# Performance work log

Measured on AMD Instinct MI355X. Metric: run time of the kernel, lower is better.

Reference implementation:

```python
import jax, jax.numpy as jnp
import numpy as np
from jax import lax

ANCHOR_AREAS = (128.0**2, 256.0**2, 512.0**2)
ASPECT_RATIOS = (0.5, 1.0, 2.0)
STRIDE = 32.0                      # resnet backbone: get_orig_stat maps fm -> input via x*32
PRE_NMS_TOP_N = 2000
POST_NMS_TOP_N = 100
NMS_IOU_T = 0.7
SCORE_T = 0.1
MIN_SCALE = 0.01
BBOX_XFORM_CLIP = float(np.log(1000.0 / 16.0))


def make_anchors(H, W):
    # anchors laid out in (H, W, A) order to match the offset permutation below
    sizes = []
    for area in ANCHOR_AREAS:
        for r in ASPECT_RATIOS:          # aspect_ratio = w / h
            sizes.append((np.sqrt(area * r), np.sqrt(area / r)))
    sizes = jnp.asarray(np.asarray(sizes, dtype=np.float32))  # [A, 2] (w, h)
    cy = (jnp.arange(H, dtype=jnp.float32) + 0.5) * STRIDE
    cx = (jnp.arange(W, dtype=jnp.float32) + 0.5) * STRIDE
    cyg, cxg = jnp.meshgrid(cy, cx, indexing='ij')             # [H, W]
    cxg = cxg[:, :, None]
    cyg = cyg[:, :, None]
    w = sizes[:, 0]
    h = sizes[:, 1]
    anchors = jnp.stack([cxg - w / 2, cyg - h / 2, cxg + w / 2, cyg + h / 2], axis=-1)
    return anchors.reshape(-1, 4)                              # [H*W*A, 4] xyxy


def decode_boxes(anchors, offsets):
    # anchors [N,4], offsets [B,N,4] (tx, ty, tw, th) -> boxes [B,N,4] xyxy
    wa = anchors[:, 2] - anchors[:, 0]
    ha = anchors[:, 3] - anchors[:, 1]
    cxa = anchors[:, 0] + 0.5 * wa
    cya = anchors[:, 1] + 0.5 * ha
    tx, ty = offsets[..., 0], offsets[..., 1]
    tw = jnp.minimum(offsets[..., 2], BBOX_XFORM_CLIP)
    th = jnp.minimum(offsets[..., 3], BBOX_XFORM_CLIP)
    px = tx * wa + cxa
    py = ty * ha + cya
    pw = jnp.exp(tw) * wa
    ph = jnp.exp(th) * ha
    return jnp.stack([px - pw / 2, py - ph / 2, px + pw / 2, py + ph / 2], axis=-1)


def box_iou(a, b):
    area_a = (a[:, 2] - a[:, 0]) * (a[:, 3] - a[:, 1])
    area_b = (b[:, 2] - b[:, 0]) * (b[:, 3] - b[:, 1])
    lt = jnp.maximum(a[:, None, :2], b[None, :, :2])
    rb = jnp.minimum(a[:, None, 2:], b[None, :, 2:])
    wh = jnp.clip(rb - lt, 0.0)
    inter = wh[..., 0] * wh[..., 1]
    return inter / (area_a[:, None] + area_b[None, :] - inter + 1e-9)


def nms_single(boxes, scores):
    # boxes [P,4] sorted by descending score; invalid entries carry score -1
    P = boxes.shape[0]
    iou = box_iou(boxes, boxes)
    idx = jnp.arange(P)

    def body(i, keep):
        sup = (iou[i] > NMS_IOU_T) & (idx > i)
        return jnp.where(keep[i], keep & (~sup), keep)

    keep = lax.stop_gradient(lax.fori_loop(0, P, body, scores > 0.0))
    kept_scores = jnp.where(keep, scores, -1.0)
    top_s, top_i = lax.top_k(kept_scores, POST_NMS_TOP_N)
    return boxes[top_i], top_s


def rpn_forward(features, W1, b1, W2, b2, W3, b3):
    B, Cin, H, W = features.shape
    A = W3.shape[0]
    # 3x3 sliding conv + ReLU
    t = lax.conv_general_dilated(
        features, W1, window_strides=(1, 1), padding='SAME',
        dimension_numbers=('NCHW', 'OIHW', 'NCHW'))
    t = jax.nn.relu(t + b1[None, :, None, None])
    # 1x1 sibling heads as channel contractions
    offs = jnp.einsum('bchw,oc->bohw', t, W2) + b2[None, :, None, None]   # [B, A*4, H, W]
    logits = jnp.einsum('bchw,oc->bohw', t, W3) + b3[None, :, None, None]  # [B, A, H, W]
    # reorder to per-anchor layout (H, W, A)
    offs = offs.reshape(B, A, 4, H, W).transpose(0, 3, 4, 1, 2).reshape(B, -1, 4)
    scores = jax.nn.sigmoid(logits.transpose(0, 2, 3, 1).reshape(B, -1))  # [B, N]
    anchors = make_anchors(H, W)
    boxes = decode_boxes(anchors, offs)                                    # [B, N, 4]
    # clip to image boundary (handle_cross_boundary_boxes during testing)
    img_w, img_h = W * STRIDE, H * STRIDE
    boxes = jnp.stack([
        jnp.clip(boxes[..., 0], 0.0, img_w),
        jnp.clip(boxes[..., 1], 0.0, img_h),
        jnp.clip(boxes[..., 2], 0.0, img_w),
        jnp.clip(boxes[..., 3], 0.0, img_h)], axis=-1)
    # score-threshold + min-scale filtering
    bw = boxes[..., 2] - boxes[..., 0]
    bh = boxes[..., 3] - boxes[..., 1]
    valid = (scores >= SCORE_T) & (bw > MIN_SCALE * img_w) & (bh > MIN_SCALE * img_h)
    masked = jnp.where(valid, scores, -1.0)
    # pre-NMS top-k, then per-image NMS + post-NMS top-n
    top_s, top_i = lax.top_k(masked, PRE_NMS_TOP_N)                        # [B, P]
    top_boxes = jnp.take_along_axis(boxes, top_i[..., None], axis=1)       # [B, P, 4]
    out_boxes, out_scores = jax.vmap(nms_single)(top_boxes, top_s)
    return out_boxes, out_scores                                           # [B,100,4], [B,100]


def setup_inputs() -> dict:
    key = jax.random.key(0)
    ks = jax.random.split(key, 4)
    B, Cin, H, W = 8, 1024, 50, 50
    A = 9
    C = 512
    return {
        'features': jax.random.normal(ks[0], (B, Cin, H, W), jnp.float32),
        'W1': jax.random.normal(ks[1], (C, Cin, 3, 3), jnp.float32) * 0.01,
        'b1': jnp.zeros((C,), jnp.float32),
        'W2': jax.random.normal(ks[2], (A * 4, C), jnp.float32) * 0.01,
        'b2': jnp.zeros((A * 4,), jnp.float32),
        'W3': jax.random.normal(ks[3], (A, C), jnp.float32) * 0.01,
        'b3': jnp.zeros((A,), jnp.float32),
    }


def reference(features, W1, b1, W2, b2, W3, b3):
    return rpn_forward(features, W1, b1, W2, b2, W3, b3)
```

## Files before the change

kernel.cpp:

```cpp
#include <hip/hip_runtime.h>
#include <cstdint>

#define NB 8
#define CIN 1024
#define HDIM 50
#define WDIM 50
#define COUT 512
#define NA 9
#define NANCH (HDIM*WDIM*NA)
#define PRE_N 2000
#define POST_N 100

typedef __attribute__((ext_vector_type(8))) short bf16x8;
typedef __attribute__((ext_vector_type(4))) float f32x4;
typedef __attribute__((ext_vector_type(16))) float f32x16;
typedef __attribute__((ext_vector_type(8))) unsigned short ushort8v;

constexpr size_t TPLANE    = 20578304;
constexpr size_t OFF_TPH   = 0;
constexpr size_t OFF_TPL   = 20578304;
constexpr size_t OFF_BOXES = 41156608;
constexpr size_t OFF_KEYS  = 44036608;
constexpr size_t OFF_TBOX  = 45476608;
constexpr size_t OFF_TS    = 45732608;
constexpr size_t OFF_SUP   = 45796608;
constexpr size_t QDIM      = 2976;
constexpr size_t PLSTRIDE  = QDIM * 8;
constexpr size_t PPLANE    = 48758784;
constexpr size_t OFF_PH    = 49892864;
constexpr size_t OFF_PL    = OFF_PH + PPLANE;
constexpr size_t WPLANE    = 9437184;
constexpr size_t OFF_WH    = 147410432;
constexpr size_t OFF_WL    = OFF_WH + WPLANE;

__device__ __forceinline__ void split2bf16(float v, unsigned short &hi, unsigned short &lo) {
    unsigned int u = __float_as_uint(v);
    unsigned int r = u + 0x7FFFu + ((u >> 16) & 1u);
    hi = (unsigned short)(r >> 16);
    float hf = __uint_as_float(((unsigned int)hi) << 16);
    float lf = v - hf;
    unsigned int u2 = __float_as_uint(lf);
    unsigned int r2 = u2 + 0x7FFFu + ((u2 >> 16) & 1u);
    lo = (unsigned short)(r2 >> 16);
}

__device__ __forceinline__ void gl_lds(const unsigned short* g, unsigned short* l) {
    __builtin_amdgcn_global_load_lds(
        (const __attribute__((address_space(1))) unsigned int*)(const void*)g,
        (__attribute__((address_space(3))) unsigned int*)(void*)l,
        16, 0, 0);
}

__global__ __launch_bounds__(256) void prep_all(const float* __restrict__ f,
                                                const float* __restrict__ W1,
                                                unsigned short* __restrict__ Ph,
                                                unsigned short* __restrict__ Pl,
                                                unsigned short* __restrict__ Wh,
                                                unsigned short* __restrict__ Wl) {
    int blk = blockIdx.x;
    if (blk < 5952) {
        int id = blk * 256 + threadIdx.x;
        int q = id % (int)QDIM; int r = id / (int)QDIM;
        int cic = r % 64; int b = r / 64;
        int pp = q - 53;
        int rr = pp / 52, cc = pp - rr * 52;
        int h = rr - 1, w = cc - 1;
        bool inb = (pp >= 0) && (pp < 2704) && (h >= 0) && (h < HDIM) && (w >= 0) && (w < WDIM);
        ushort8v hv0, lv0, hv1, lv1;
#pragma unroll
        for (int j = 0; j < 16; ++j) {
            float v = 0.f;
            if (inb) v = f[(((size_t)b * CIN + cic * 16 + j) * HDIM + h) * WDIM + w];
            unsigned short hi, lo;
            split2bf16(v, hi, lo);
            if (j < 8) { hv0[j] = hi; lv0[j] = lo; }
            else       { hv1[j - 8] = hi; lv1[j - 8] = lo; }
        }
        size_t b0 = ((size_t)((b * 64 + cic) * 2 + 0)) * PLSTRIDE + (size_t)q * 8;
        size_t b1 = ((size_t)((b * 64 + cic) * 2 + 1)) * PLSTRIDE + (size_t)q * 8;
        *(ushort8v*)&Ph[b0] = hv0;
        *(ushort8v*)&Ph[b1] = hv1;
        *(ushort8v*)&Pl[b0] = lv0;
        *(ushort8v*)&Pl[b1] = lv1;
    } else {
        int id = (blk - 5952) * 256 + threadIdx.x;
        int co = id % 64; int r = id / 64;
        int cic = r % 64; int cot = r / 64;
        int cog = cot * 64 + co;
        const float* src = W1 + ((size_t)cog * CIN + cic * 16) * 9;
        float v[144];
#pragma unroll
        for (int i = 0; i < 36; ++i) {
            float4 x = ((const float4*)src)[i];
            v[i * 4 + 0] = x.x; v[i * 4 + 1] = x.y; v[i * 4 + 2] = x.z; v[i * 4 + 3] = x.w;
        }
#pragma unroll
        for (int tap = 0; tap < 9; ++tap) {
            ushort8v hv0, lv0, hv1, lv1;
#pragma unroll
            for (int j = 0; j < 16; ++j) {
                unsigned short hi, lo;
                split2bf16(v[j * 9 + tap], hi, lo);
                if (j < 8) { hv0[j] = hi; lv0[j] = lo; }
                else       { hv1[j - 8] = hi; lv1[j - 8] = lo; }
            }
            size_t base = (((size_t)(cot * 64 + cic) * 9 + tap) * 2) * 512;
            *(ushort8v*)&Wh[base + co * 8]       = hv0;
            *(ushort8v*)&Wh[base + 512 + co * 8] = hv1;
            *(ushort8v*)&Wl[base + co * 8]       = lv0;
            *(ushort8v*)&Wl[base + 512 + co * 8] = lv1;
        }
    }
}


#define LOADA(SET_, SRC_, TG_)                                                       \
    do {                                                                             \
        _Pragma("unroll") for (int tl_ = 0; tl_ < 3; ++tl_) {                        \
            const int dlt_ = ((TG_) - 1) * 52 + (tl_ - 1);                           \
            _Pragma("unroll") for (int jm_ = 0; jm_ < 2; ++jm_) {                    \
                int ad_ = ((wv * 2 + jm_) * 32 + lm + dlt_ + 53) * 8;                \
                SET_[tl_][jm_][0] = *(const bf16x8*)&(SRC_)[lk * 3072 + ad_];        \
                SET_[tl_][jm_][1] = *(const bf16x8*)&(SRC_)[(2 + lk) * 3072 + ad_];  \
            }                                                                        \
        }                                                                            \
    } while (0)

#define LOADB(B_, BB_, TL_)                                                          \
    do {                                                                             \
        _Pragma("unroll") for (int jn_ = 0; jn_ < 2; ++jn_) {                        \
            int bd_ = (TL_) * 1024 + lk * 512 + (jn_ * 32 + lm) * 8;                 \
            B_[jn_][0] = *(const bf16x8*)&(BB_)[bd_];                                \
            B_[jn_][1] = *(const bf16x8*)&(BB_)[3072 + bd_];                         \
        }                                                                            \
    } while (0)

#define MFMA12A(SET_, TL_, B_)                                                       \
    do {                                                                             \
        _Pragma("unroll") for (int s_ = 0; s_ < 3; ++s_)                             \
        _Pragma("unroll") for (int jm_ = 0; jm_ < 2; ++jm_)                          \
        _Pragma("unroll") for (int jn_ = 0; jn_ < 2; ++jn_) {                        \
            const bf16x8 &av_ = (s_ == 2) ? SET_[TL_][jm_][1] : SET_[TL_][jm_][0];   \
            const bf16x8 &bv_ = (s_ == 1) ? B_[jn_][1] : B_[jn_][0];                 \
            acc[jm_][jn_] = __builtin_amdgcn_mfma_f32_32x32x16_bf16(                 \
                av_, bv_, acc[jm_][jn_], 0, 0, 0);                                   \
        }                                                                            \
    } while (0)

#define PHASE(CUR_, NXT_, CIC_, TG_, PRESRC_, NTG_, STAGEON_)                        \
    do {                                                                             \
        const int bbuf_ = ((CIC_) + (TG_)) & 1;                                      \
        const unsigned short* bB_ = Bbase + bbuf_ * 6144;                            \
        if ((STAGEON_) || (TG_) < 2) {                                               \
            int cicb_ = ((TG_) == 2) ? (CIC_) + 1 : (CIC_);                          \
            int tgn_  = ((TG_) == 2) ? 0 : (TG_) + 1;                                \
            _Pragma("unroll") for (int j_ = 0; j_ < 3; ++j_)                         \
                stageB(bbuf_ ^ 1, cicb_, tgn_, wv * 3 + j_);                         \
        }                                                                            \
        if (STAGEON_) {                                                              \
            if ((TG_) == 0) {                                                        \
                _Pragma("unroll") for (int j_ = 0; j_ < 3; ++j_)                     \
                    stageA((((CIC_) & 1) ^ 1), (CIC_) + 1, wv * 3 + j_);             \
            } else if ((TG_) == 1) {                                                 \
                _Pragma("unroll") for (int j_ = 0; j_ < 2; ++j_)                     \
                    stageA((((CIC_) & 1) ^ 1), (CIC_) + 1, 12 + wv * 2 + j_);        \
            } else {                                                                 \
                stageA((((CIC_) & 1) ^ 1), (CIC_) + 1, 20 + wv);                     \
            }                                                                        \
        }                                                                            \
        bf16x8 b0_[2][2], b1_[2][2];                                                 \
        LOADB(b0_, bB_, 0);                                                          \
        __builtin_amdgcn_s_setprio(1);                                               \
        LOADB(b1_, bB_, 1);                                                          \
        MFMA12A(CUR_, 0, b0_);                                                       \
        LOADB(b0_, bB_, 2);                                                          \
        if ((STAGEON_) || (TG_) < 2) LOADA(NXT_, PRESRC_, NTG_);                     \
        MFMA12A(CUR_, 1, b1_);                                                       \
        MFMA12A(CUR_, 2, b0_);                                                       \
        __builtin_amdgcn_s_setprio(0);                                               \
        if (STAGEON_) {                                                              \
            const int nv_ = ((TG_) == 0) ? 6 : ((TG_) == 1) ? 5 : 4;                 \
            __builtin_amdgcn_sched_group_barrier(0x070, nv_, 0);                     \
            __builtin_amdgcn_sched_group_barrier(0x100, 8, 0);                       \
            _Pragma("unroll") for (int g_ = 0; g_ < 8; ++g_) {                       \
                __builtin_amdgcn_sched_group_barrier(0x008, 3, 0);                   \
                __builtin_amdgcn_sched_group_barrier(0x100, 2, 0);                   \
            }                                                                        \
            __builtin_amdgcn_sched_group_barrier(0x008, 12, 0);                      \
        }                                                                            \
        __syncthreads();                                                             \
    } while (0)

#define DO_CIC(CUR_, NXT_, CIC_, STAGEON_)                                           \
    do {                                                                             \
        const unsigned short* bAc_ = Abase + ((CIC_) & 1) * 12288;                   \
        const unsigned short* bAn_ = Abase + (((CIC_) & 1) ^ 1) * 12288;             \
        PHASE(CUR_, NXT_, CIC_, 0, bAc_, 1, STAGEON_);                               \
        PHASE(NXT_, CUR_, CIC_, 1, bAc_, 2, STAGEON_);                               \
        PHASE(CUR_, NXT_, CIC_, 2, bAn_, 0, STAGEON_);                               \
    } while (0)

__global__ __launch_bounds__(256, 2) void conv_mfma(const unsigned short* __restrict__ FPh,
                                                    const unsigned short* __restrict__ FPl,
                                                    const unsigned short* __restrict__ WPh,
                                                    const unsigned short* __restrict__ WPl,
                                                    const float* __restrict__ b1,
                                                    unsigned short* __restrict__ Tph,
                                                    unsigned short* __restrict__ Tpl) {
    extern __shared__ unsigned short smem[];
    unsigned short* const Abase = smem;
    unsigned short* const Bbase = smem + 24576;

    int blk = blockIdx.x;
    int logical = (blk & 7) * 88 + (blk >> 3);
    int cot = logical & 7;
    int ptile = (logical >> 3) % 11;
    int b = logical / 88;
    int co0 = cot * 64;
    int P0 = 32 + ptile * 256;

    int t = threadIdx.x, wv = t >> 6, ln = t & 63;
    int lm = ln & 31, lk = ln >> 5;

    f32x16 acc[2][2];
#pragma unroll
    for (int jm = 0; jm < 2; ++jm)
#pragma unroll
        for (int jn = 0; jn < 2; ++jn)
#pragma unroll
            for (int rg = 0; rg < 16; ++rg) acc[jm][jn][rg] = 0.f;

    auto stageA = [&](int buf, int cic, int ci) {
        int r = (ci < 20) ? (ci & 3) : (ci - 20);
        int s = (ci < 20) ? (ci >> 2) : 5;
        int hl = r >> 1, lkc = r & 1;
        const unsigned short* pl = hl ? FPl : FPh;
        const unsigned short* src = pl
            + ((size_t)((b * 64 + cic) * 2 + lkc)) * PLSTRIDE
            + (size_t)P0 * 8 + s * 512 + ln * 8;
        gl_lds(src, &Abase[buf * 12288 + r * 3072 + s * 512]);
    };
    auto stageB = [&](int buf, int cic, int tg, int c) {
        int hl = c / 6, j = c % 6;
        const unsigned short* pl = hl ? WPl : WPh;
        const unsigned short* src = pl + (size_t)(cot * 64 + cic) * 9216
            + (size_t)(tg * 6 + j) * 512 + ln * 8;
        gl_lds(src, &Bbase[buf * 6144 + hl * 3072 + j * 512]);
    };

#pragma unroll
    for (int k = 0; k < 9; ++k) {
        int id = wv * 9 + k;
        if (id < 24) stageA(0, 0, id);
        else         stageB(0, 0, 0, id - 24);
    }
    __syncthreads();

    bf16x8 aX[3][2][2], aY[3][2][2];
    LOADA(aX, Abase, 0);

#pragma unroll 1
    for (int cc = 0; cc < 31; ++cc) {
        DO_CIC(aX, aY, 2 * cc,     1);
        DO_CIC(aY, aX, 2 * cc + 1, 1);
    }
    DO_CIC(aX, aY, 62, 1);
    DO_CIC(aY, aX, 63, 0);

#pragma unroll
    for (int jn = 0; jn < 2; ++jn) {
        int co = co0 + jn * 32 + lm;
        float bv = b1[co];
#pragma unroll
        for (int jm = 0; jm < 2; ++jm) {
#pragma unroll
            for (int rg = 0; rg < 16; ++rg) {
                int mrow = (rg & 3) + 8 * (rg >> 2) + 4 * lk;
                int pp = P0 + (wv * 2 + jm) * 32 + mrow;
                int rr = pp / 52, cc = pp - rr * 52;
                int h = rr - 1, w = cc - 1;
                if ((unsigned)h < HDIM && (unsigned)w < WDIM) {
                    float v = fmaxf(acc[jm][jn][rg] + bv, 0.f);
                    unsigned short hi, lo;
                    split2bf16(v, hi, lo);
                    int px = b * 2500 + h * 50 + w;
                    size_t sa = (((((size_t)(px >> 7) * 16 + (co >> 5)) * 8 + ((px >> 4) & 7)) * 4
                                  + ((co >> 3) & 3)) * 16 + (px & 15)) * 8 + (co & 7);
                    Tph[sa] = hi;
                    Tpl[sa] = lo;
                }
            }
        }
    }
}

__global__ __launch_bounds__(256) void proj_decode_mfma(const unsigned short* __restrict__ Tph,
                                                        const unsigned short* __restrict__ Tpl,
                                                        const float* __restrict__ W2,
                                                        const float* __restrict__ b2,
                                                        const float* __restrict__ W3,
                                                        const float* __restrict__ b3,
                                                        float* __restrict__ boxes,
                                                        unsigned long long* __restrict__ keys) {
    __shared__ unsigned short sTh[4096], sTl[4096];
    __shared__ unsigned short sWh[1536], sWl[1536];
    __shared__ float pout[128 * 46];

    int blk = blockIdx.x;
    int px0 = blk * 128;
    int t = threadIdx.x, wv = t >> 6, ln = t & 63;
    int lm = ln & 15, q = ln >> 4;

    f32x4 acc[2][3];
#pragma unroll
    for (int jm = 0; jm < 2; ++jm)
#pragma unroll
        for (int nf = 0; nf < 3; ++nf) acc[jm][nf] = (f32x4){0.f, 0.f, 0.f, 0.f};

#pragma unroll 1
    for (int cc16 = 0; cc16 < 16; ++cc16) {
        __syncthreads();
        size_t base = ((size_t)blk * 16 + cc16) * 4096;
        if (wv == 0) {
#pragma unroll
            for (int s = 0; s < 4; ++s) gl_lds(Tph + base + s * 512 + ln * 8, &sTh[s * 512]);
        } else if (wv == 1) {
#pragma unroll
            for (int s = 4; s < 8; ++s) gl_lds(Tph + base + s * 512 + ln * 8, &sTh[s * 512]);
        } else if (wv == 2) {
#pragma unroll
            for (int s = 0; s < 4; ++s) gl_lds(Tpl + base + s * 512 + ln * 8, &sTl[s * 512]);
        } else {
#pragma unroll
            for (int s = 4; s < 8; ++s) gl_lds(Tpl + base + s * 512 + ln * 8, &sTl[s * 512]);
        }
        int c0 = cc16 * 32;
        for (int idx = t; idx < 1536; idx += 256) {
            int o = idx >> 5, ci = idx & 31;
            float v = 0.f;
            if (o < 36) v = W2[o * 512 + c0 + ci];
            else if (o < 45) v = W3[(o - 36) * 512 + c0 + ci];
            unsigned short hi, lo;
            split2bf16(v, hi, lo);
            int ad = (((o >> 4) * 4 + (ci >> 3)) * 16 + (o & 15)) * 8 + (ci & 7);
            sWh[ad] = hi; sWl[ad] = lo;
        }
        __syncthreads();

        bf16x8 a[2][2], bb[3][2];
#pragma unroll
        for (int jm = 0; jm < 2; ++jm) {
            int mf = wv * 2 + jm;
            int ad = ((mf * 4 + q) * 16 + lm) * 8;
            a[jm][0] = *(const bf16x8*)&sTh[ad];
            a[jm][1] = *(const bf16x8*)&sTl[ad];
        }
#pragma unroll
        for (int nf = 0; nf < 3; ++nf) {
            int ad = ((nf * 4 + q) * 16 + lm) * 8;
            bb[nf][0] = *(const bf16x8*)&sWh[ad];
            bb[nf][1] = *(const bf16x8*)&sWl[ad];
        }
#pragma unroll
        for (int jm = 0; jm < 2; ++jm)
#pragma unroll
            for (int nf = 0; nf < 3; ++nf) {
                acc[jm][nf] = __builtin_amdgcn_mfma_f32_16x16x32_bf16(a[jm][0], bb[nf][0], acc[jm][nf], 0, 0, 0);
                acc[jm][nf] = __builtin_amdgcn_mfma_f32_16x16x32_bf16(a[jm][0], bb[nf][1], acc[jm][nf], 0, 0, 0);
                acc[jm][nf] = __builtin_amdgcn_mfma_f32_16x16x32_bf16(a[jm][1], bb[nf][0], acc[jm][nf], 0, 0, 0);
            }
    }
    __syncthreads();
#pragma unroll
    for (int jm = 0; jm < 2; ++jm)
#pragma unroll
        for (int nf = 0; nf < 3; ++nf) {
            int o = nf * 16 + lm;
            if (o < 45) {
                float bias = (o < 36) ? b2[o] : b3[o - 36];
#pragma unroll
                for (int rg = 0; rg < 4; ++rg) {
                    int pxl = (wv * 2 + jm) * 16 + q * 4 + rg;
                    pout[pxl * 46 + o] = acc[jm][nf][rg] + bias;
                }
            }
        }
    __syncthreads();

    const float AW[9] = {90.50966799187809f, 128.0f, 181.01933598375618f,
                         181.01933598375618f, 256.0f, 362.03867196751236f,
                         362.03867196751236f, 512.0f, 724.0773439350247f};
    const float AH[9] = {181.01933598375618f, 128.0f, 90.50966799187809f,
                         362.03867196751236f, 256.0f, 181.01933598375618f,
                         724.0773439350247f, 512.0f, 362.03867196751236f};
    const float CLIPV = 4.135166556742356f;
    const float IMG = 1600.0f;

    for (int it = t; it < 128 * 9; it += 256) {
        int pxl = it / 9, a = it - pxl * 9;
        int pxg = px0 + pxl;
        if (pxg >= 20000) continue;
        int b = pxg / 2500, rem = pxg % 2500;
        int h = rem / 50, w = rem % 50;

        float tx = pout[pxl * 46 + a * 4 + 0];
        float ty = pout[pxl * 46 + a * 4 + 1];
        float tw = pout[pxl * 46 + a * 4 + 2];
        float th = pout[pxl * 46 + a * 4 + 3];
        float lg = pout[pxl * 46 + 36 + a];

        float s = 1.0f / (1.0f + expf(-lg));

        float cx = ((float)w + 0.5f) * 32.0f;
        float cy = ((float)h + 0.5f) * 32.0f;
        float x1a = cx - 0.5f * AW[a];
        float x2a = cx + 0.5f * AW[a];
        float y1a = cy - 0.5f * AH[a];
        float y2a = cy + 0.5f * AH[a];
        float waf = x2a - x1a;
        float haf = y2a - y1a;
        float cxa = x1a + 0.5f * waf;
        float cya = y1a + 0.5f * haf;

        float twc = tw < CLIPV ? tw : CLIPV;
        float thc = th < CLIPV ? th : CLIPV;
        float pxc = tx * waf + cxa;
        float pyc = ty * haf + cya;
        float pw  = expf(twc) * waf;
        float ph  = expf(thc) * haf;

        float x1 = pxc - 0.5f * pw;
        float y1 = pyc - 0.5f * ph;
        float x2 = pxc + 0.5f * pw;
        float y2 = pyc + 0.5f * ph;
        x1 = fminf(fmaxf(x1, 0.f), IMG);
        y1 = fminf(fmaxf(y1, 0.f), IMG);
        x2 = fminf(fmaxf(x2, 0.f), IMG);
        y2 = fminf(fmaxf(y2, 0.f), IMG);

        float bw = x2 - x1, bh = y2 - y1;
        bool valid = (s >= 0.1f) && (bw > 16.0f) && (bh > 16.0f);
        float m = valid ? s : -1.0f;

        int idx = (h * WDIM + w) * NA + a;
        size_t gi = (size_t)b * NANCH + idx;
        ((float4*)boxes)[gi] = make_float4(x1, y1, x2, y2);
        unsigned int u = __float_as_uint(m);
        unsigned int k32 = (u & 0x80000000u) ? ~u : (u | 0x80000000u);
        keys[gi] = ((unsigned long long)k32 << 15) | (unsigned long long)(32767 - idx);
    }
}

__global__ __launch_bounds__(1024) void select_sort_kernel(const unsigned long long* __restrict__ keys,
                                                           const float* __restrict__ boxes,
                                                           float* __restrict__ top_boxes,
                                                           float* __restrict__ top_s) {
    int b = blockIdx.x;
    int t = threadIdx.x;
    int wv = t >> 6;
    const unsigned long long* kb = keys + (size_t)b * NANCH;

    __shared__ unsigned int whist[16][256];
    __shared__ unsigned int hist[256];
    __shared__ int s_chosen, s_rnew, s_done;
    __shared__ unsigned int s_cnt;
    __shared__ unsigned long long skeys[2048];

    const int widths[6] = {8, 8, 8, 8, 8, 7};
    unsigned long long prefix = 0;
    int bitsdone = 0;
    int r = PRE_N;

    if (t == 0) s_done = 0;

    for (int p = 0; p < 6; ++p) {
        int width = widths[p];
        int bins = 1 << width;
        int shift = 47 - bitsdone - width;
        for (int i = t; i < 16 * 256; i += 1024) ((unsigned int*)whist)[i] = 0;
        __syncthreads();
        for (int i = t; i < NANCH; i += 1024) {
            unsigned long long k = kb[i];
            if ((k >> (47 - bitsdone)) == prefix)
                atomicAdd(&whist[wv][(unsigned)((k >> shift) & (unsigned long long)(bins - 1))], 1u);
        }
        __syncthreads();
        if (t < bins) {
            unsigned int s = 0;
#pragma unroll
            for (int w = 0; w < 16; ++w) s += whist[w][t];
            hist[t] = s;
        }
        __syncthreads();
        if (t == 0) {
            int acc = 0, chosen = 0, rnew = 1;
            for (int d = bins - 1; d >= 0; --d) {
                int hv = (int)hist[d];
                if (acc + hv >= r) {
                    chosen = d; rnew = r - acc;
                    if ((PRE_N - r) + acc + hv <= 2048) s_done = 1;
                    break;
                }
                acc += hv;
            }
            s_chosen = chosen;
            s_rnew = rnew;
        }
        __syncthreads();
        prefix = (prefix << width) | (unsigned long long)s_chosen;
        bitsdone += width;
        r = s_rnew;
        __syncthreads();
        if (s_done) break;
    }
    unsigned long long Kst = prefix << (47 - bitsdone);

    if (t == 0) s_cnt = 0;
    __syncthreads();
    for (int i = t; i < NANCH; i += 1024) {
        unsigned long long k = kb[i];
        if (k >= Kst) {
            unsigned int p = atomicAdd(&s_cnt, 1u);
            if (p < 2048) skeys[p] = k;
        }
    }
    __syncthreads();
    unsigned int cnt = s_cnt;
    for (int i = t; i < 2048; i += 1024)
        if (i >= (int)cnt) skeys[i] = 0ull;
    for (int k = 2; k <= 2048; k <<= 1) {
        for (int j = k >> 1; j > 0; j >>= 1) {
            __syncthreads();
            for (int i = t; i < 2048; i += 1024) {
                int l = i ^ j;
                if (l > i) {
                    unsigned long long a = skeys[i], c = skeys[l];
                    bool up = ((i & k) == 0);
                    if (up ? (a < c) : (a > c)) { skeys[i] = c; skeys[l] = a; }
                }
            }
        }
    }
    __syncthreads();
    for (int i = t; i < PRE_N; i += 1024) {
        unsigned long long k = skeys[i];
        unsigned int k32 = (unsigned int)(k >> 15);
        float m = (k32 & 0x80000000u) ? __uint_as_float(k32 & 0x7FFFFFFFu)
                                      : __uint_as_float(~k32);
        unsigned int idx = 32767u - (unsigned int)(k & 32767ull);
        size_t gi = (size_t)b * NANCH + idx;
        top_s[b * PRE_N + i] = m;
        ((float4*)top_boxes)[b * PRE_N + i] = ((const float4*)boxes)[gi];
    }
}

__global__ __launch_bounds__(256) void sup_kernel(const float* __restrict__ top_boxes,
                                                  unsigned long long* __restrict__ supm) {
    int blk = blockIdx.x;
    int b = blk / 125;
    int chunk = blk % 125;
    int t = threadIdx.x;

    __shared__ float bx1[PRE_N], by1[PRE_N], bx2[PRE_N], by2[PRE_N];
    for (int i = t; i < PRE_N; i += 256) {
        float4 v = ((const float4*)top_boxes)[b * PRE_N + i];
        bx1[i] = v.x; by1[i] = v.y; bx2[i] = v.z; by2[i] = v.w;
    }
    __syncthreads();

    int wave = t >> 6, lane = t & 63;
    for (int rr = 0; rr < 4; ++rr) {
        int i = chunk * 16 + wave * 4 + rr;
        float ax1 = bx1[i], ay1 = by1[i], ax2 = bx2[i], ay2 = by2[i];
        float aarea = (ax2 - ax1) * (ay2 - ay1);
        for (int jw = 0; jw < 32; ++jw) {
            int j = jw * 64 + lane;
            bool sup = false;
            if (j > i && j < PRE_N) {
                float jx1 = bx1[j], jy1 = by1[j], jx2 = bx2[j], jy2 = by2[j];
                float ix1 = fmaxf(ax1, jx1), iy1 = fmaxf(ay1, jy1);
                float ix2 = fminf(ax2, jx2), iy2 = fminf(ay2, jy2);
                float iw = fmaxf(ix2 - ix1, 0.f);
                float ih = fmaxf(iy2 - iy1, 0.f);
                float inter = iw * ih;
                float barea = (jx2 - jx1) * (jy2 - jy1);
                float iou = inter / (aarea + barea - inter + 1e-9f);
                sup = iou > 0.7f;
            }
            unsigned long long m = __ballot(sup);
            if (lane == 0) supm[((size_t)b * PRE_N + i) * 32 + jw] = m;
        }
    }
}

__global__ __launch_bounds__(256) void nms_fin_kernel(const float* __restrict__ top_s,
                                                      const unsigned long long* __restrict__ supm,
                                                      const float* __restrict__ top_boxes,
                                                      float* __restrict__ out) {
    int b = blockIdx.x;
    int t = threadIdx.x;
    __shared__ unsigned int kw[64];
    __shared__ int wpre[65];

    if (t < 64) {
        int lane = t;
        unsigned int alive = 0;
        for (int q = 0; q < 32; ++q) {
            int i = lane * 32 + q;
            if (i < PRE_N && top_s[b * PRE_N + i] > 0.f) alive |= (1u << q);
        }
        const unsigned long long* sm = supm + (size_t)b * PRE_N * 32;
        const unsigned int* sup32 = (const unsigned int*)sm;

        for (int tt = 0; tt < 32; ++tt) {
            unsigned int alo = __shfl(alive, 2 * tt);
            unsigned int ahi = __shfl(alive, 2 * tt + 1);
            unsigned long long talive = (unsigned long long)alo | ((unsigned long long)ahi << 32);
            int i_row = tt * 64 + lane;
            unsigned long long rm = (i_row < PRE_N) ? sm[(size_t)i_row * 32 + tt] : 0ull;

            unsigned long long kept = 0, rem = talive;
            while (rem) {
                int j = __builtin_ctzll(rem);
                kept |= (1ull << j);
                unsigned long long rmj = __shfl(rm, j);
                rem &= ~rmj;
                rem &= ~(1ull << j);
            }

            unsigned int oracc = 0;
            unsigned long long kk = kept;
            while (kk) {
                int j0 = __builtin_ctzll(kk); kk &= kk - 1;
                int j1 = -1, j2 = -1, j3 = -1, j4 = -1, j5 = -1, j6 = -1, j7 = -1;
                if (kk) { j1 = __builtin_ctzll(kk); kk &= kk - 1; }
                if (kk) { j2 = __builtin_ctzll(kk); kk &= kk - 1; }
                if (kk) { j3 = __builtin_ctzll(kk); kk &= kk - 1; }
                if (kk) { j4 = __builtin_ctzll(kk); kk &= kk - 1; }
                if (kk) { j5 = __builtin_ctzll(kk); kk &= kk - 1; }
                if (kk) { j6 = __builtin_ctzll(kk); kk &= kk - 1; }
                if (kk) { j7 = __builtin_ctzll(kk); kk &= kk - 1; }
                unsigned int v0 = sup32[(size_t)(tt * 64 + j0) * 64 + lane];
                unsigned int v1 = (j1 >= 0) ? sup32[(size_t)(tt * 64 + j1) * 64 + lane] : 0u;
                unsigned int v2 = (j2 >= 0) ? sup32[(size_t)(tt * 64 + j2) * 64 + lane] : 0u;
                unsigned int v3 = (j3 >= 0) ? sup32[(size_t)(tt * 64 + j3) * 64 + lane] : 0u;
                unsigned int v4 = (j4 >= 0) ? sup32[(size_t)(tt * 64 + j4) * 64 + lane] : 0u;
                unsigned int v5 = (j5 >= 0) ? sup32[(size_t)(tt * 64 + j5) * 64 + lane] : 0u;
                unsigned int v6 = (j6 >= 0) ? sup32[(size_t)(tt * 64 + j6) * 64 + lane] : 0u;
                unsigned int v7 = (j7 >= 0) ? sup32[(size_t)(tt * 64 + j7) * 64 + lane] : 0u;
                oracc |= (v0 | v1) | (v2 | v3) | (v4 | v5) | (v6 | v7);
            }
            alive &= ~oracc;
            if (lane == 2 * tt)     alive = (unsigned int)kept;
            if (lane == 2 * tt + 1) alive = (unsigned int)(kept >> 32);
        }
        kw[lane] = alive;
    }
    __syncthreads();
    if (t == 0) {
        int run = 0;
        for (int w = 0; w < 64; ++w) { wpre[w] = run; run += __popc(kw[w]); }
        wpre[64] = run;
    }
    __syncthreads();
    int total = wpre[64];
    float* out_boxes  = out;
    float* out_scores = out + NB * POST_N * 4;
    for (int i = t; i < PRE_N; i += 256) {
        unsigned int w = kw[i >> 5];
        bool kept = (w >> (i & 31)) & 1u;
        int rk = wpre[i >> 5] + __popc(w & ((1u << (i & 31)) - 1u));
        int pos = kept ? rk : total + (i - rk);
        if (pos < POST_N) {
            out_scores[b * POST_N + pos] = kept ? top_s[b * PRE_N + i] : -1.0f;
            ((float4*)out_boxes)[b * POST_N + pos] = ((const float4*)top_boxes)[b * PRE_N + i];
        }
    }
}

extern "C" void kernel_launch(void* const* d_in, const int* in_sizes, int n_in,
                              void* d_out, int out_size, void* d_ws, size_t ws_size,
                              hipStream_t stream) {
    const float* features = (const float*)d_in[0];
    const float* W1 = (const float*)d_in[1];
    const float* b1 = (const float*)d_in[2];
    const float* W2 = (const float*)d_in[3];
    const float* b2 = (const float*)d_in[4];
    const float* W3 = (const float*)d_in[5];
    const float* b3 = (const float*)d_in[6];
    float* out = (float*)d_out;
    char* ws = (char*)d_ws;

    unsigned short* Tph = (unsigned short*)(ws + OFF_TPH);
    unsigned short* Tpl = (unsigned short*)(ws + OFF_TPL);
    float* boxes   = (float*)(ws + OFF_BOXES);
    unsigned long long* keys = (unsigned long long*)(ws + OFF_KEYS);
    float* top_boxes = (float*)(ws + OFF_TBOX);
    float* top_s     = (float*)(ws + OFF_TS);
    unsigned long long* supm = (unsigned long long*)(ws + OFF_SUP);
    unsigned short* FPh = (unsigned short*)(ws + OFF_PH);
    unsigned short* FPl = (unsigned short*)(ws + OFF_PL);
    unsigned short* WPh = (unsigned short*)(ws + OFF_WH);
    unsigned short* WPl = (unsigned short*)(ws + OFF_WL);

    static bool conv_attr_set = false;
    if (!conv_attr_set) {
        hipFuncSetAttribute(reinterpret_cast<const void*>(&conv_mfma),
                            hipFuncAttributeMaxDynamicSharedMemorySize, 73728);
        conv_attr_set = true;
    }

    prep_all<<<6080, 256, 0, stream>>>(features, W1, FPh, FPl, WPh, WPl);
    conv_mfma<<<704, 256, 73728, stream>>>(FPh, FPl, WPh, WPl, b1, Tph, Tpl);
    proj_decode_mfma<<<157, 256, 0, stream>>>(Tph, Tpl, W2, b2, W3, b3, boxes, keys);
    select_sort_kernel<<<NB, 1024, 0, stream>>>(keys, boxes, top_boxes, top_s);
    sup_kernel<<<NB * 125, 256, 0, stream>>>(top_boxes, supm);
    nms_fin_kernel<<<NB, 256, 0, stream>>>(top_s, supm, top_boxes, out);
}
```

Before: 973.7 us.

## Load conv weights directly from global into registers, drop LDS staging of B

```diff
diff --git a/kernel.cpp b/kernel.cpp
--- a/kernel.cpp
+++ b/kernel.cpp
@@ -126,15 +126,6 @@
         }                                                                            \
     } while (0)
 
-#define LOADB(B_, BB_, TL_)                                                          \
-    do {                                                                             \
-        _Pragma("unroll") for (int jn_ = 0; jn_ < 2; ++jn_) {                        \
-            int bd_ = (TL_) * 1024 + lk * 512 + (jn_ * 32 + lm) * 8;                 \
-            B_[jn_][0] = *(const bf16x8*)&(BB_)[bd_];                                \
-            B_[jn_][1] = *(const bf16x8*)&(BB_)[3072 + bd_];                         \
-        }                                                                            \
-    } while (0)
-
 #define MFMA12A(SET_, TL_, B_)                                                       \
     do {                                                                             \
         _Pragma("unroll") for (int s_ = 0; s_ < 3; ++s_)                             \
@@ -147,57 +138,45 @@
         }                                                                            \
     } while (0)
 
-#define PHASE(CUR_, NXT_, CIC_, TG_, PRESRC_, NTG_, STAGEON_)                        \
+#define PHASEV(CUR_, NXT_, CIC_, TG_, PRESRC_, NTG_, DOA_, DOLOADA_)                 \
     do {                                                                             \
-        const int bbuf_ = ((CIC_) + (TG_)) & 1;                                      \
-        const unsigned short* bB_ = Bbase + bbuf_ * 6144;                            \
-        if ((STAGEON_) || (TG_) < 2) {                                               \
-            int cicb_ = ((TG_) == 2) ? (CIC_) + 1 : (CIC_);                          \
-            int tgn_  = ((TG_) == 2) ? 0 : (TG_) + 1;                                \
+        size_t wo_ = (size_t)(cot * 64 + (CIC_)) * 9216 + (size_t)((TG_) * 3072);    \
+        bf16x8 bb_[3][2][2];                                                         \
+        _Pragma("unroll") for (int tl_ = 0; tl_ < 3; ++tl_)                          \
+        _Pragma("unroll") for (int jn_ = 0; jn_ < 2; ++jn_) {                        \
+            size_t o_ = wo_ + (size_t)(tl_ * 1024 + lk * 512 + (jn_ * 32 + lm) * 8); \
+            bb_[tl_][jn_][0] = *(const bf16x8*)&WPh[o_];                             \
+            bb_[tl_][jn_][1] = *(const bf16x8*)&WPl[o_];                             \
+        }                                                                            \
+        if (DOA_) {                                                                  \
             _Pragma("unroll") for (int j_ = 0; j_ < 3; ++j_)                         \
-                stageB(bbuf_ ^ 1, cicb_, tgn_, wv * 3 + j_);                         \
+                stageA(abn_, (CIC_) + 1, (TG_) * 12 + wv * 3 + j_);                  \
         }                                                                            \
-        if (STAGEON_) {                                                              \
-            if ((TG_) == 0) {                                                        \
-                _Pragma("unroll") for (int j_ = 0; j_ < 3; ++j_)                     \
-                    stageA((((CIC_) & 1) ^ 1), (CIC_) + 1, wv * 3 + j_);             \
-            } else if ((TG_) == 1) {                                                 \
-                _Pragma("unroll") for (int j_ = 0; j_ < 2; ++j_)                     \
-                    stageA((((CIC_) & 1) ^ 1), (CIC_) + 1, 12 + wv * 2 + j_);        \
-            } else {                                                                 \
-                stageA((((CIC_) & 1) ^ 1), (CIC_) + 1, 20 + wv);                     \
+        __builtin_amdgcn_s_setprio(1);                                               \
+        MFMA12A(CUR_, 0, bb_[0]);                                                    \
+        if (DOLOADA_) LOADA(NXT_, PRESRC_, NTG_);                                    \
+        MFMA12A(CUR_, 1, bb_[1]);                                                    \
+        MFMA12A(CUR_, 2, bb_[2]);                                                    \
+        __builtin_amdgcn_s_setprio(0);                                               \
+        if (DOLOADA_) {                                                              \
+                                         \
+            __builtin_amdgcn_sched_group_barrier(0x070, (DOA_) ? 27 : 24, 0);        \
+            _Pragma("unroll") for (int g_ = 0; g_ < 12; ++g_) {                      \
+                __builtin_amdgcn_sched_group_barrier(0x008, 3, 0);                   \
+                __builtin_amdgcn_sched_group_barrier(0x100, 1, 0);                   \
             }                                                                        \
         }                                                                            \
-        bf16x8 b0_[2][2], b1_[2][2];                                                 \
-        LOADB(b0_, bB_, 0);                                                          \
-        __builtin_amdgcn_s_setprio(1);                                               \
-        LOADB(b1_, bB_, 1);                                                          \
-        MFMA12A(CUR_, 0, b0_);                                                       \
-        LOADB(b0_, bB_, 2);                                                          \
-        if ((STAGEON_) || (TG_) < 2) LOADA(NXT_, PRESRC_, NTG_);                     \
-        MFMA12A(CUR_, 1, b1_);                                                       \
-        MFMA12A(CUR_, 2, b0_);                                                       \
-        __builtin_amdgcn_s_setprio(0);                                               \
-        if (STAGEON_) {                                                              \
-            const int nv_ = ((TG_) == 0) ? 6 : ((TG_) == 1) ? 5 : 4;                 \
-            __builtin_amdgcn_sched_group_barrier(0x070, nv_, 0);                     \
-            __builtin_amdgcn_sched_group_barrier(0x100, 8, 0);                       \
-            _Pragma("unroll") for (int g_ = 0; g_ < 8; ++g_) {                       \
-                __builtin_amdgcn_sched_group_barrier(0x008, 3, 0);                   \
-                __builtin_amdgcn_sched_group_barrier(0x100, 2, 0);                   \
-            }                                                                        \
-            __builtin_amdgcn_sched_group_barrier(0x008, 12, 0);                      \
-        }                                                                            \
-        __syncthreads();                                                             \
     } while (0)
 
-#define DO_CIC(CUR_, NXT_, CIC_, STAGEON_)                                           \
+#define DO_CICV(CUR_, NXT_, CIC_, STAGEON_, LOADLAST_)                               \
     do {                                                                             \
         const unsigned short* bAc_ = Abase + ((CIC_) & 1) * 12288;                   \
         const unsigned short* bAn_ = Abase + (((CIC_) & 1) ^ 1) * 12288;             \
-        PHASE(CUR_, NXT_, CIC_, 0, bAc_, 1, STAGEON_);                               \
-        PHASE(NXT_, CUR_, CIC_, 1, bAc_, 2, STAGEON_);                               \
-        PHASE(CUR_, NXT_, CIC_, 2, bAn_, 0, STAGEON_);                               \
+        const int abn_ = ((CIC_) & 1) ^ 1;                                           \
+        PHASEV(CUR_, NXT_, CIC_, 0, bAc_, 1, STAGEON_, 1);                           \
+        PHASEV(NXT_, CUR_, CIC_, 1, bAc_, 2, STAGEON_, 1);                           \
+        __syncthreads();                                                             \
+        PHASEV(CUR_, NXT_, CIC_, 2, bAn_, 0, 0, LOADLAST_);                          \
     } while (0)
 
 __global__ __launch_bounds__(256, 2) void conv_mfma(const unsigned short* __restrict__ FPh,
@@ -207,9 +186,8 @@
                                                     const float* __restrict__ b1,
                                                     unsigned short* __restrict__ Tph,
                                                     unsigned short* __restrict__ Tpl) {
-    extern __shared__ unsigned short smem[];
-    unsigned short* const Abase = smem;
-    unsigned short* const Bbase = smem + 24576;
+    __shared__ unsigned short sA[2][4][3072];
+    unsigned short* const Abase = &sA[0][0][0];
 
     int blk = blockIdx.x;
     int logical = (blk & 7) * 88 + (blk >> 3);
@@ -231,8 +209,7 @@
             for (int rg = 0; rg < 16; ++rg) acc[jm][jn][rg] = 0.f;
 
     auto stageA = [&](int buf, int cic, int ci) {
-        int r = (ci < 20) ? (ci & 3) : (ci - 20);
-        int s = (ci < 20) ? (ci >> 2) : 5;
+        int r = ci & 3, s = ci >> 2;
         int hl = r >> 1, lkc = r & 1;
         const unsigned short* pl = hl ? FPl : FPh;
         const unsigned short* src = pl
@@ -240,20 +217,9 @@
             + (size_t)P0 * 8 + s * 512 + ln * 8;
         gl_lds(src, &Abase[buf * 12288 + r * 3072 + s * 512]);
     };
-    auto stageB = [&](int buf, int cic, int tg, int c) {
-        int hl = c / 6, j = c % 6;
-        const unsigned short* pl = hl ? WPl : WPh;
-        const unsigned short* src = pl + (size_t)(cot * 64 + cic) * 9216
-            + (size_t)(tg * 6 + j) * 512 + ln * 8;
-        gl_lds(src, &Bbase[buf * 6144 + hl * 3072 + j * 512]);
-    };
-
-#pragma unroll
-    for (int k = 0; k < 9; ++k) {
-        int id = wv * 9 + k;
-        if (id < 24) stageA(0, 0, id);
-        else         stageB(0, 0, 0, id - 24);
-    }
+
+#pragma unroll
+    for (int k = 0; k < 6; ++k) stageA(0, 0, wv * 6 + k);
     __syncthreads();
 
     bf16x8 aX[3][2][2], aY[3][2][2];
@@ -261,11 +227,11 @@
 
 #pragma unroll 1
     for (int cc = 0; cc < 31; ++cc) {
-        DO_CIC(aX, aY, 2 * cc,     1);
-        DO_CIC(aY, aX, 2 * cc + 1, 1);
-    }
-    DO_CIC(aX, aY, 62, 1);
-    DO_CIC(aY, aX, 63, 0);
+        DO_CICV(aX, aY, 2 * cc,     1, 1);
+        DO_CICV(aY, aX, 2 * cc + 1, 1, 1);
+    }
+    DO_CICV(aX, aY, 62, 1, 1);
+    DO_CICV(aY, aX, 63, 0, 0);
 
 #pragma unroll
     for (int jn = 0; jn < 2; ++jn) {
@@ -703,15 +669,8 @@
     unsigned short* WPh = (unsigned short*)(ws + OFF_WH);
     unsigned short* WPl = (unsigned short*)(ws + OFF_WL);
 
-    static bool conv_attr_set = false;
-    if (!conv_attr_set) {
-        hipFuncSetAttribute(reinterpret_cast<const void*>(&conv_mfma),
-                            hipFuncAttributeMaxDynamicSharedMemorySize, 73728);
-        conv_attr_set = true;
-    }
-
     prep_all<<<6080, 256, 0, stream>>>(features, W1, FPh, FPl, WPh, WPl);
-    conv_mfma<<<704, 256, 73728, stream>>>(FPh, FPl, WPh, WPl, b1, Tph, Tpl);
+    conv_mfma<<<704, 256, 0, stream>>>(FPh, FPl, WPh, WPl, b1, Tph, Tpl);
     proj_decode_mfma<<<157, 256, 0, stream>>>(Tph, Tpl, W2, b2, W3, b3, boxes, keys);
     select_sort_kernel<<<NB, 1024, 0, stream>>>(keys, boxes, top_boxes, top_s);
     sup_kernel<<<NB * 125, 256, 0, stream>>>(top_boxes, supm);
```

Result: slower. 1.063 ms (+9.2%).
